# Optimization experiments

Measured on AMD Instinct MI355X. Metric: run time of the kernel, lower is better.

The kernel has to match this reference:

```python
import jax, jax.numpy as jnp
import numpy as np

T = 10.0            # neuralef_loss_cfg['t']
ALPHA = 0.05        # neuralef_loss_cfg['alpha']
PW_W = 0.1          # pixelwise_adj_weight
PW_DIV = 1.0        # pixelwise_adj_div_factor
K_LIST = ((20, 2.0), (10, 0.1))  # hard-coded in source


def _pdist(x):
    # x: (b, n, d) -> (b, n, n) euclidean distance (torch.cdist)
    sq = jnp.sum(x * x, -1)
    d2 = sq[:, :, None] + sq[:, None, :] - 2.0 * jnp.einsum('bnd,bmd->bnm', x, x)
    return jnp.sqrt(jnp.maximum(d2, 0.0))


def _mutual_knn(feats, k):
    # mutual k-NN boolean adjacency: scatter topk then AND with transpose
    bs, n, _ = feats.shape
    neg = -_pdist(feats)
    neg = jnp.where(jnp.eye(n, dtype=bool), -jnp.inf, neg)
    idx = jax.lax.top_k(neg, k)[1]                       # (bs, n, k)
    res = jnp.zeros((bs, n, n), dtype=bool).at[
        jnp.arange(bs)[:, None, None], jnp.arange(n)[None, :, None], idx].set(True)
    return jnp.logical_and(res, res.transpose(0, 2, 1))


def setup_inputs() -> dict:
    key = jax.random.key(0)
    k1, k2, k3 = jax.random.split(key, 3)
    N, C, K = 8192, 384, 512
    bs, h, w = 8, 32, 32
    FF = jax.random.normal(k1, (N, C), dtype=jnp.float32)
    Psi = jax.random.normal(k2, (N, K), dtype=jnp.float32)
    im = jax.random.uniform(k3, (bs, 3, h, w), dtype=jnp.float32, minval=-1.0, maxval=1.0)
    return {"FF": FF, "Psi": Psi, "im": im}


def reference(FF, Psi, im):
    N = FF.shape[0]
    Psi = Psi * (T / N)
    # --- adjacency (torch.no_grad block) ---
    FFn = FF / jnp.linalg.norm(FF, axis=1, keepdims=True)
    A = FFn @ FFn.T
    A = jnp.where(jnp.eye(N, dtype=bool), 0.0, A)       # fill_diagonal_(0)
    A = jnp.maximum(A, 0.0)                              # thresholded kernel
    # --- pixelwise mutual-kNN adjacency per image ---
    bs, _, h, w = im.shape
    hw = h * w
    im01 = (im + 1.0) * 0.5
    x_ = jnp.tile(jnp.linspace(0.0, 1.0, w), h)          # (hw,)
    y_ = jnp.repeat(jnp.linspace(0.0, 1.0, h), w)        # (hw,)
    feat = im01.reshape(bs, 3, hw).transpose(0, 2, 1) / PW_DIV  # (bs, hw, 3)
    A_p = None
    for k, dw in K_LIST:
        f2 = jnp.concatenate([
            feat,
            jnp.broadcast_to((x_ * dw)[None, :, None], (bs, hw, 1)),
            jnp.broadcast_to((y_ * dw)[None, :, None], (bs, hw, 1)),
        ], -1)
        m = _mutual_knn(f2, k)
        A_p = m if A_p is None else jnp.logical_or(A_p, m)
    # add PW_W * A_p to block-diagonal blocks of A
    A4 = A.reshape(bs, hw, bs, hw)
    bi = jnp.arange(bs)
    A4 = A4.at[bi, :, bi, :].add(PW_W * A_p.astype(A.dtype))
    A = A4.reshape(N, N)
    # degree normalization
    D = jax.lax.rsqrt(A.sum(-1) / (N - 1))
    gram = A * D[None, :] * D[:, None]
    # --- neuralef loss ---
    R = Psi.T @ gram @ Psi                               # (K, K)
    R_hat = jax.lax.stop_gradient(Psi).T @ gram @ Psi    # no_sg=False
    loss = -jnp.trace(R)
    reg = jnp.sum(jnp.triu(R_hat ** 2, 1)) * ALPHA
    return jnp.stack([loss, reg])
```

## Files before the change

### kernel.cpp

```cpp
#include <hip/hip_runtime.h>
#include <hip/hip_bf16.h>

#define NN 8192
#define CC 384
#define KD 512
#define HWP 1024

typedef __attribute__((ext_vector_type(8))) short bf16x8;
typedef __attribute__((ext_vector_type(4))) float f32x4;

static constexpr float T_OVER_N = 10.0f / 8192.0f;

__device__ __forceinline__ float bf2f(unsigned short u) {
    union { unsigned int i; float f; } x;
    x.i = ((unsigned int)u) << 16;
    return x.f;
}
__device__ __forceinline__ unsigned short f2bf(float f) {
    __hip_bfloat16 h = __float2bfloat16(f);
    unsigned short u;
    __builtin_memcpy(&u, &h, sizeof(u));
    return u;
}

__device__ __forceinline__ void wait_vm8() {
    asm volatile("s_waitcnt vmcnt(8)" ::: "memory");
    __builtin_amdgcn_sched_barrier(0);
}
__device__ __forceinline__ void wait_vm0() {
    asm volatile("s_waitcnt vmcnt(0)" ::: "memory");
    __builtin_amdgcn_sched_barrier(0);
}
__device__ __forceinline__ void rawbar() {
    __builtin_amdgcn_s_barrier();
    __builtin_amdgcn_sched_barrier(0);
}

__device__ __forceinline__ void stage_tile(const unsigned short* __restrict__ src, long ld,
                                           int k0, unsigned short* lds) {
    const int t = threadIdx.x;
    #pragma unroll
    for (int i = 0; i < 4; ++i) {
        int slot = i * 256 + t;
        int row = slot >> 3;
        int cl = (slot & 7) ^ (row & 7);
        const unsigned short* g = src + (long)row * ld + k0 + cl * 8;
        __builtin_amdgcn_global_load_lds((const __attribute__((address_space(1))) void*)g,
                                         (__attribute__((address_space(3))) void*)(lds + (size_t)slot * 8),
                                         16, 0, 0);
    }
}

__device__ __forceinline__ bf16x8 read_frag(const unsigned short* lds, int r, int chunk) {
    int byte = (r << 7) + (((chunk ^ r) & 7) << 4) + ((chunk & ~7) << 4);
    return *(const bf16x8*)((const char*)lds + byte);
}

__device__ __forceinline__ void gemm_step(const unsigned short* As, const unsigned short* Bs,
                                          int arl, int brl, int lhi, f32x4 (&acc)[4][4]) {
    #pragma unroll
    for (int ks = 0; ks < 2; ++ks) {
        bf16x8 a[4], b[4];
        #pragma unroll
        for (int m = 0; m < 4; ++m) a[m] = read_frag(As, arl + m * 16, ks * 4 + lhi);
        #pragma unroll
        for (int n = 0; n < 4; ++n) b[n] = read_frag(Bs, brl + n * 16, ks * 4 + lhi);
        #pragma unroll
        for (int m = 0; m < 4; ++m)
            #pragma unroll
            for (int n = 0; n < 4; ++n)
                acc[m][n] = __builtin_amdgcn_mfma_f32_16x16x32_bf16(a[m], b[n], acc[m][n], 0, 0, 0);
    }
}

__global__ __launch_bounds__(128) void k_normalize(const float* __restrict__ FF,
                                                   unsigned short* __restrict__ FFnb) {
    int row = blockIdx.x;
    int tid = threadIdx.x;
    const float* src = FF + (size_t)row * CC;
    float v0 = src[tid], v1 = src[tid + 128], v2 = src[tid + 256];
    float s = v0 * v0 + v1 * v1 + v2 * v2;
    #pragma unroll
    for (int off = 32; off > 0; off >>= 1) s += __shfl_down(s, off, 64);
    __shared__ float ls[2];
    if ((tid & 63) == 0) ls[tid >> 6] = s;
    __syncthreads();
    float inv = 1.0f / sqrtf(ls[0] + ls[1]);
    unsigned short* dst = FFnb + (size_t)row * CC;
    dst[tid] = f2bf(v0 * inv);
    dst[tid + 128] = f2bf(v1 * inv);
    dst[tid + 256] = f2bf(v2 * inv);
}

__global__ __launch_bounds__(256) void k_knn(const float* __restrict__ im,
                                             unsigned char* __restrict__ res20,
                                             unsigned char* __restrict__ res10) {
    const int lane = threadIdx.x & 63;
    const int id = blockIdx.x * 4 + (threadIdx.x >> 6);
    const int v = id & 1;
    const int rest = id >> 1;
    const int p = rest & 1023;
    const int b = rest >> 10;
    const float dw = v ? 0.1f : 2.0f;
    const int kneigh = v ? 10 : 20;
    const float* im0 = im + (size_t)b * 3 * HWP;
    const float scale = dw * (1.0f / 31.0f);
    float rf0 = (im0[p] + 1.f) * 0.5f;
    float rf1 = (im0[HWP + p] + 1.f) * 0.5f;
    float rf2 = (im0[2 * HWP + p] + 1.f) * 0.5f;
    float rx = (float)(p & 31) * scale;
    float ry = (float)(p >> 5) * scale;
    unsigned int key[16];
    #pragma unroll
    for (int e = 0; e < 16; ++e) {
        int q = e * 64 + lane;
        float f0 = (im0[q] + 1.f) * 0.5f - rf0;
        float f1 = (im0[HWP + q] + 1.f) * 0.5f - rf1;
        float f2 = (im0[2 * HWP + q] + 1.f) * 0.5f - rf2;
        float fx = (float)(q & 31) * scale - rx;
        float fy = (float)(q >> 5) * scale - ry;
        float d = f0 * f0 + f1 * f1 + f2 * f2 + fx * fx + fy * fy;
        unsigned int db = __float_as_uint(d);
        key[e] = (q == p) ? 0xFFFFFFFFu : ((db & 0xFFFFFC00u) | (unsigned int)q);
    }
    unsigned int selmask = 0;
    for (int it = 0; it < kneigh; ++it) {
        unsigned int m = key[0];
        #pragma unroll
        for (int e = 1; e < 16; ++e) m = (key[e] < m) ? key[e] : m;
        #pragma unroll
        for (int off = 1; off < 64; off <<= 1) {
            unsigned int o = __shfl_xor(m, off, 64);
            m = (o < m) ? o : m;
        }
        int q = (int)(m & 1023u);
        if ((q & 63) == lane) {
            int e = q >> 6;
            selmask |= 1u << e;
            key[e] = 0xFFFFFFFFu;
        }
    }
    unsigned char* dst = (v ? res10 : res20) + ((size_t)(b * HWP + p)) * HWP;
    #pragma unroll
    for (int e = 0; e < 16; ++e) dst[e * 64 + lane] = (unsigned char)((selmask >> e) & 1u);
}

__global__ __launch_bounds__(256, 2) void k_gram_off(const unsigned short* __restrict__ FFnb,
                                                     unsigned short* __restrict__ A,
                                                     float* __restrict__ rowsum) {
    __shared__ __align__(16) unsigned short Sh[4][8192];
    int s = ((blockIdx.x & 7) * 260) + (blockIdx.x >> 3);
    int ti = 0, rem = s;
    while (rem >= 64 - ti) { rem -= 64 - ti; ++ti; }
    const int tj = ti + rem;
    if ((ti >> 3) == (tj >> 3)) return;
    const int row0 = ti * 128, col0 = tj * 128;
    const int tid = threadIdx.x, l = tid & 63, wid = tid >> 6;
    const int wr = (wid >> 1) * 64, wc = (wid & 1) * 64;
    const int arl = wr + (l & 15), brl = wc + (l & 15), lhi = l >> 4;
    f32x4 z = {0.f, 0.f, 0.f, 0.f};
    f32x4 acc[4][4];
    #pragma unroll
    for (int m = 0; m < 4; ++m)
        #pragma unroll
        for (int n = 0; n < 4; ++n) acc[m][n] = z;

    stage_tile(FFnb + (long)row0 * CC, CC, 0, Sh[0]);
    stage_tile(FFnb + (long)col0 * CC, CC, 0, Sh[1]);
    for (int t = 0; t < 6; ++t) {
        const int cur = t & 1, nxt = cur ^ 1;
        if (t + 1 < 6) {
            stage_tile(FFnb + (long)row0 * CC, CC, (t + 1) * 64, Sh[2 * nxt]);
            stage_tile(FFnb + (long)col0 * CC, CC, (t + 1) * 64, Sh[2 * nxt + 1]);
            wait_vm8();
        } else {
            wait_vm0();
        }
        rawbar();
        gemm_step(Sh[2 * cur], Sh[2 * cur + 1], arl, brl, lhi, acc);
        rawbar();
    }
    float rs[4][4];
    float cs[4] = {0.f, 0.f, 0.f, 0.f};
    #pragma unroll
    for (int m = 0; m < 4; ++m)
        #pragma unroll
        for (int r = 0; r < 4; ++r) rs[m][r] = 0.f;
    char* Mir = (char*)Sh;
    #pragma unroll
    for (int m = 0; m < 4; ++m) {
        #pragma unroll
        for (int n = 0; n < 4; ++n) {
            #pragma unroll
            for (int r = 0; r < 4; ++r) {
                int il = wr + m * 16 + lhi * 4 + r;
                int jl = wc + n * 16 + (l & 15);
                float vv = fmaxf(acc[m][n][r], 0.f);
                unsigned short u = f2bf(vv);
                A[(long)(row0 + il) * NN + col0 + jl] = u;
                rs[m][r] += vv;
                cs[n] += vv;
                *(unsigned short*)(Mir + jl * 256 + ((il * 2) ^ ((jl & 15) << 4))) = u;
            }
        }
    }
    #pragma unroll
    for (int m = 0; m < 4; ++m)
        #pragma unroll
        for (int r = 0; r < 4; ++r) {
            float p = rs[m][r];
            #pragma unroll
            for (int off = 1; off < 16; off <<= 1) p += __shfl_xor(p, off, 64);
            if ((l & 15) == 0) atomicAdd(&rowsum[row0 + wr + m * 16 + lhi * 4 + r], p);
        }
    #pragma unroll
    for (int n = 0; n < 4; ++n) {
        float p = cs[n];
        p += __shfl_xor(p, 16, 64);
        p += __shfl_xor(p, 32, 64);
        if (l < 16) atomicAdd(&rowsum[col0 + wc + n * 16 + l], p);
    }
    __syncthreads();
    #pragma unroll
    for (int p8 = 0; p8 < 8; ++p8) {
        int idx = p8 * 256 + tid;
        int jl = idx >> 4;
        int cl = idx & 15;
        int sl = cl ^ (jl & 15);
        bf16x8 v = *(const bf16x8*)(Mir + jl * 256 + sl * 16);
        *(bf16x8*)(A + (long)(col0 + jl) * NN + row0 + cl * 8) = v;
    }
}

__global__ __launch_bounds__(256, 2) void k_gram_diag(const unsigned short* __restrict__ FFnb,
                                                      const unsigned char* __restrict__ res20,
                                                      const unsigned char* __restrict__ res10,
                                                      unsigned short* __restrict__ A,
                                                      float* __restrict__ rowsum) {
    __shared__ __align__(16) unsigned short Sh[4][8192];
    int s = ((blockIdx.x & 7) * 36) + (blockIdx.x >> 3);
    int band = s / 36, p = s % 36;
    int a = 0, rem = p;
    while (rem >= 8 - a) { rem -= 8 - a; ++a; }
    const int ti = band * 8 + a, tj = band * 8 + a + rem;
    const int row0 = ti * 128, col0 = tj * 128;
    const int tid = threadIdx.x, l = tid & 63, wid = tid >> 6;
    const int wr = (wid >> 1) * 64, wc = (wid & 1) * 64;
    const int arl = wr + (l & 15), brl = wc + (l & 15), lhi = l >> 4;
    f32x4 z = {0.f, 0.f, 0.f, 0.f};
    f32x4 acc[4][4];
    #pragma unroll
    for (int m = 0; m < 4; ++m)
        #pragma unroll
        for (int n = 0; n < 4; ++n) acc[m][n] = z;

    stage_tile(FFnb + (long)row0 * CC, CC, 0, Sh[0]);
    stage_tile(FFnb + (long)col0 * CC, CC, 0, Sh[1]);
    for (int t = 0; t < 6; ++t) {
        const int cur = t & 1, nxt = cur ^ 1;
        if (t + 1 < 6) {
            stage_tile(FFnb + (long)row0 * CC, CC, (t + 1) * 64, Sh[2 * nxt]);
            stage_tile(FFnb + (long)col0 * CC, CC, (t + 1) * 64, Sh[2 * nxt + 1]);
            wait_vm8();
        } else {
            wait_vm0();
        }
        rawbar();
        gemm_step(Sh[2 * cur], Sh[2 * cur + 1], arl, brl, lhi, acc);
        rawbar();
    }
    const bool offd = (ti != tj);
    const long mbase = ((long)band) << 20;
    float rs[4][4];
    float cs[4] = {0.f, 0.f, 0.f, 0.f};
    #pragma unroll
    for (int m = 0; m < 4; ++m)
        #pragma unroll
        for (int r = 0; r < 4; ++r) rs[m][r] = 0.f;
    char* Mir = (char*)Sh;
    #pragma unroll
    for (int m = 0; m < 4; ++m) {
        #pragma unroll
        for (int n = 0; n < 4; ++n) {
            #pragma unroll
            for (int r = 0; r < 4; ++r) {
                int il = wr + m * 16 + lhi * 4 + r;
                int jl = wc + n * 16 + (l & 15);
                int gi = row0 + il, gj = col0 + jl;
                float vv = acc[m][n][r];
                vv = (gi == gj) ? 0.f : fmaxf(vv, 0.f);
                int li = gi & 1023, lj = gj & 1023;
                unsigned char mm = (unsigned char)(
                    (res20[mbase + (long)li * HWP + lj] & res20[mbase + (long)lj * HWP + li]) |
                    (res10[mbase + (long)li * HWP + lj] & res10[mbase + (long)lj * HWP + li]));
                vv += 0.1f * (float)mm;
                unsigned short u = f2bf(vv);
                A[(long)gi * NN + gj] = u;
                rs[m][r] += vv;
                if (offd) {
                    cs[n] += vv;
                    *(unsigned short*)(Mir + jl * 256 + ((il * 2) ^ ((jl & 15) << 4))) = u;
                }
            }
        }
    }
    #pragma unroll
    for (int m = 0; m < 4; ++m)
        #pragma unroll
        for (int r = 0; r < 4; ++r) {
            float p2 = rs[m][r];
            #pragma unroll
            for (int off = 1; off < 16; off <<= 1) p2 += __shfl_xor(p2, off, 64);
            if ((l & 15) == 0) atomicAdd(&rowsum[row0 + wr + m * 16 + lhi * 4 + r], p2);
        }
    if (offd) {
        #pragma unroll
        for (int n = 0; n < 4; ++n) {
            float p2 = cs[n];
            p2 += __shfl_xor(p2, 16, 64);
            p2 += __shfl_xor(p2, 32, 64);
            if (l < 16) atomicAdd(&rowsum[col0 + wc + n * 16 + l], p2);
        }
        __syncthreads();
        #pragma unroll
        for (int p8 = 0; p8 < 8; ++p8) {
            int idx = p8 * 256 + tid;
            int jl = idx >> 4;
            int cl = idx & 15;
            int sl = cl ^ (jl & 15);
            bf16x8 v = *(const bf16x8*)(Mir + jl * 256 + sl * 16);
            *(bf16x8*)(A + (long)(col0 + jl) * NN + row0 + cl * 8) = v;
        }
    }
}

__global__ __launch_bounds__(256) void k_d(const float* __restrict__ rowsum,
                                           float* __restrict__ Dv) {
    int i = blockIdx.x * 256 + threadIdx.x;
    Dv[i] = 1.0f / sqrtf(rowsum[i] * (1.0f / 8191.0f));
}

__global__ __launch_bounds__(256) void k_psiT(const float* __restrict__ Psi,
                                              const float* __restrict__ Dv,
                                              unsigned short* __restrict__ PaT,
                                              unsigned short* __restrict__ PsT) {
    __shared__ unsigned short tile[128][72];
    __shared__ float Dvs[64];
    const int j0 = blockIdx.x * 64;
    const int n0 = blockIdx.y * 128;
    const int t = threadIdx.x;
    if (t < 64) Dvs[t] = Dv[j0 + t];
    #pragma unroll
    for (int i = 0; i < 8; ++i) {
        int jl = i * 8 + (t >> 5);
        int c4 = (t & 31) * 4;
        float4 vv = *(const float4*)(Psi + (size_t)(j0 + jl) * KD + n0 + c4);
        tile[c4 + 0][jl] = f2bf(vv.x * T_OVER_N);
        tile[c4 + 1][jl] = f2bf(vv.y * T_OVER_N);
        tile[c4 + 2][jl] = f2bf(vv.z * T_OVER_N);
        tile[c4 + 3][jl] = f2bf(vv.w * T_OVER_N);
    }
    __syncthreads();
    const int nl = t >> 1;
    const int jh = (t & 1) * 32;
    unsigned short pa[32], ps[32];
    #pragma unroll
    for (int jj = 0; jj < 32; ++jj) {
        unsigned short u = tile[nl][jh + jj];
        pa[jj] = u;
        ps[jj] = f2bf(bf2f(u) * Dvs[jh + jj]);
    }
    unsigned short* dpa = PaT + (size_t)(n0 + nl) * NN + j0 + jh;
    unsigned short* dps = PsT + (size_t)(n0 + nl) * NN + j0 + jh;
    #pragma unroll
    for (int c = 0; c < 4; ++c) {
        *(bf16x8*)(dpa + c * 8) = *(const bf16x8*)(pa + c * 8);
        *(bf16x8*)(dps + c * 8) = *(const bf16x8*)(ps + c * 8);
    }
}

__global__ __launch_bounds__(256, 2) void k_yt5(const unsigned short* __restrict__ A,
                                                const unsigned short* __restrict__ PsT,
                                                unsigned short* __restrict__ Wpart) {
    __shared__ __align__(16) unsigned short Sh[4][8192];
    int slot = (blockIdx.x & 7) * 64 + (blockIdx.x >> 3);
    const int it = slot >> 3;
    const int sub = slot & 7;
    const int nt = sub & 3, kz = sub >> 2;
    const int row0 = it * 128, col0 = nt * 128;
    const int tid = threadIdx.x, l = tid & 63, wid = tid >> 6;
    const int wr = (wid >> 1) * 64, wc = (wid & 1) * 64;
    const int arl = wr + (l & 15), brl = wc + (l & 15), lhi = l >> 4;
    f32x4 z = {0.f, 0.f, 0.f, 0.f};
    f32x4 acc[4][4];
    #pragma unroll
    for (int m = 0; m < 4; ++m)
        #pragma unroll
        for (int n = 0; n < 4; ++n) acc[m][n] = z;

    const unsigned short* Abase = A + (long)row0 * NN;
    const unsigned short* Bbase = PsT + (long)col0 * NN;
    const int kbeg = kz * 4096;
    stage_tile(Abase, NN, kbeg, Sh[0]);
    stage_tile(Bbase, NN, kbeg, Sh[1]);
    for (int t = 0; t < 64; ++t) {
        const int cur = t & 1, nxt = cur ^ 1;
        if (t + 1 < 64) {
            int k1 = kbeg + (t + 1) * 64;
            stage_tile(Abase, NN, k1, Sh[2 * nxt]);
            stage_tile(Bbase, NN, k1, Sh[2 * nxt + 1]);
            wait_vm8();
        } else {
            wait_vm0();
        }
        rawbar();
        gemm_step(Sh[2 * cur], Sh[2 * cur + 1], arl, brl, lhi, acc);
        rawbar();
    }
    unsigned short* Wp = Wpart + (long)kz * NN * KD;
    #pragma unroll
    for (int m = 0; m < 4; ++m) {
        #pragma unroll
        for (int r = 0; r < 4; ++r) {
            int gi = row0 + wr + m * 16 + lhi * 4 + r;
            #pragma unroll
            for (int n = 0; n < 4; ++n) {
                int gj = col0 + wc + n * 16 + (l & 15);
                Wp[(long)gi * KD + gj] = f2bf(acc[m][n][r]);
            }
        }
    }
}

__global__ __launch_bounds__(256) void k_comb(const unsigned short* __restrict__ Wpart,
                                              const float* __restrict__ Dv,
                                              unsigned short* __restrict__ YT) {
    __shared__ unsigned short t64[64][80];
    const int i0 = blockIdx.x * 64;
    const int n0 = blockIdx.y * 64;
    const int t = threadIdx.x;
    int il = t >> 2, nc = (t & 3) * 16;
    const unsigned short* p0 = Wpart + (long)(i0 + il) * KD + n0 + nc;
    const unsigned short* p1 = p0 + (long)NN * KD;
    bf16x8 a0 = *(const bf16x8*)p0;
    bf16x8 a1 = *(const bf16x8*)(p0 + 8);
    bf16x8 b0 = *(const bf16x8*)p1;
    bf16x8 b1 = *(const bf16x8*)(p1 + 8);
    float dvi = Dv[i0 + il];
    #pragma unroll
    for (int e = 0; e < 8; ++e) {
        t64[nc + e][il]     = f2bf((bf2f((unsigned short)a0[e]) + bf2f((unsigned short)b0[e])) * dvi);
        t64[nc + 8 + e][il] = f2bf((bf2f((unsigned short)a1[e]) + bf2f((unsigned short)b1[e])) * dvi);
    }
    __syncthreads();
    int nl = t >> 2, jc = (t & 3) * 16;
    bf16x8 o0 = *(const bf16x8*)(&t64[nl][jc]);
    bf16x8 o1 = *(const bf16x8*)(&t64[nl][jc + 8]);
    *(bf16x8*)(YT + (long)(n0 + nl) * NN + i0 + jc) = o0;
    *(bf16x8*)(YT + (long)(n0 + nl) * NN + i0 + jc + 8) = o1;
}

__global__ __launch_bounds__(256, 2) void k_r(const unsigned short* __restrict__ PaT,
                                              const unsigned short* __restrict__ YT,
                                              float* __restrict__ R) {
    static const int t1tab[10] = {0,0,0,0,1,1,1,2,2,3};
    static const int t2tab[10] = {0,1,2,3,1,2,3,2,3,3};
    const int t1 = t1tab[blockIdx.x], t2 = t2tab[blockIdx.x], kz = blockIdx.y;
    __shared__ __align__(16) unsigned short Sh[4][8192];
    const int row0 = t1 * 128, col0 = t2 * 128;
    const int tid = threadIdx.x, l = tid & 63, wid = tid >> 6;
    const int wr = (wid >> 1) * 64, wc = (wid & 1) * 64;
    const int arl = wr + (l & 15), brl = wc + (l & 15), lhi = l >> 4;
    f32x4 z = {0.f, 0.f, 0.f, 0.f};
    f32x4 acc[4][4];
    #pragma unroll
    for (int m = 0; m < 4; ++m)
        #pragma unroll
        for (int n = 0; n < 4; ++n) acc[m][n] = z;

    const int kbeg = kz * 512;
    stage_tile(PaT + (long)row0 * NN, NN, kbeg, Sh[0]);
    stage_tile(YT + (long)col0 * NN, NN, kbeg, Sh[1]);
    for (int t = 0; t < 8; ++t) {
        const int cur = t & 1, nxt = cur ^ 1;
        if (t + 1 < 8) {
            int k1 = kbeg + (t + 1) * 64;
            stage_tile(PaT + (long)row0 * NN, NN, k1, Sh[2 * nxt]);
            stage_tile(YT + (long)col0 * NN, NN, k1, Sh[2 * nxt + 1]);
            wait_vm8();
        } else {
            wait_vm0();
        }
        rawbar();
        gemm_step(Sh[2 * cur], Sh[2 * cur + 1], arl, brl, lhi, acc);
        rawbar();
    }
    #pragma unroll
    for (int m = 0; m < 4; ++m) {
        #pragma unroll
        for (int n = 0; n < 4; ++n) {
            #pragma unroll
            for (int r = 0; r < 4; ++r) {
                int gk1 = row0 + wr + m * 16 + lhi * 4 + r;
                int gk2 = col0 + wc + n * 16 + (l & 15);
                atomicAdd(&R[(long)gk1 * KD + gk2], acc[m][n][r]);
            }
        }
    }
}

__global__ __launch_bounds__(256) void k_tri(const float* __restrict__ R,
                                             float* __restrict__ acc2) {
    float tr = 0.f, rg = 0.f;
    for (int idx = blockIdx.x * 256 + threadIdx.x; idx < KD * KD; idx += 64 * 256) {
        int k1 = idx >> 9, k2 = idx & 511;
        float v = R[idx];
        if (k1 == k2) tr += v;
        else if (k1 < k2) rg += v * v;
    }
    #pragma unroll
    for (int off = 32; off > 0; off >>= 1) {
        tr += __shfl_down(tr, off, 64);
        rg += __shfl_down(rg, off, 64);
    }
    __shared__ float lt[4], lr[4];
    int tid = threadIdx.x;
    if ((tid & 63) == 0) { lt[tid >> 6] = tr; lr[tid >> 6] = rg; }
    __syncthreads();
    if (tid == 0) {
        atomicAdd(&acc2[0], lt[0] + lt[1] + lt[2] + lt[3]);
        atomicAdd(&acc2[1], lr[0] + lr[1] + lr[2] + lr[3]);
    }
}

__global__ void k_fin(const float* __restrict__ acc2, float* __restrict__ out) {
    out[0] = -acc2[0];
    out[1] = 0.05f * acc2[1];
}

extern "C" void kernel_launch(void* const* d_in, const int* in_sizes, int n_in,
                              void* d_out, int out_size, void* d_ws, size_t ws_size,
                              hipStream_t stream) {
    const float* FF  = (const float*)d_in[0];
    const float* Psi = (const float*)d_in[1];
    const float* im  = (const float*)d_in[2];
    float* out = (float*)d_out;
    char* ws = (char*)d_ws;
    size_t off = 0;
    auto alloc = [&](size_t bytes) {
        size_t o = off;
        off += (bytes + 255) & ~(size_t)255;
        return o;
    };
    unsigned short* FFnb  = (unsigned short*)(ws + alloc((size_t)NN * CC * 2));
    unsigned char* res20  = (unsigned char*)(ws + alloc((size_t)8 * HWP * HWP));
    unsigned char* res10  = (unsigned char*)(ws + alloc((size_t)8 * HWP * HWP));
    float* rowsum         = (float*)(ws + alloc((size_t)NN * 4));
    float* Dv             = (float*)(ws + alloc((size_t)NN * 4));
    unsigned short* PaT   = (unsigned short*)(ws + alloc((size_t)KD * NN * 2));
    unsigned short* PsT   = (unsigned short*)(ws + alloc((size_t)KD * NN * 2));
    unsigned short* Wpart = (unsigned short*)(ws + alloc((size_t)2 * NN * KD * 2));
    unsigned short* YT    = (unsigned short*)(ws + alloc((size_t)KD * NN * 2));
    float* R              = (float*)(ws + alloc((size_t)KD * KD * 4));
    float* acc2           = (float*)(ws + alloc(256));
    unsigned short* A     = (unsigned short*)(ws + alloc((size_t)NN * NN * 2));

    hipMemsetAsync(rowsum, 0, (size_t)NN * 4, stream);
    hipMemsetAsync(R, 0, (size_t)KD * KD * 4, stream);
    hipMemsetAsync(acc2, 0, 8, stream);

    k_normalize<<<NN, 128, 0, stream>>>(FF, FFnb);
    k_knn<<<4096, 256, 0, stream>>>(im, res20, res10);
    k_gram_off<<<2080, 256, 0, stream>>>(FFnb, A, rowsum);
    k_gram_diag<<<288, 256, 0, stream>>>(FFnb, res20, res10, A, rowsum);
    k_d<<<NN / 256, 256, 0, stream>>>(rowsum, Dv);
    k_psiT<<<dim3(128, 4), 256, 0, stream>>>(Psi, Dv, PaT, PsT);
    k_yt5<<<512, 256, 0, stream>>>(A, PsT, Wpart);
    k_comb<<<dim3(NN / 64, KD / 64), 256, 0, stream>>>(Wpart, Dv, YT);
    k_r<<<dim3(10, 16), 256, 0, stream>>>(PaT, YT, R);
    k_tri<<<64, 256, 0, stream>>>(R, acc2);
    k_fin<<<1, 1, 0, stream>>>(acc2, out);
}
```

Before: 292.4 us.

## Halve gram kernel LDS to raise occupancy and stage both A tile stores

Cuts shared memory in both gram kernels from four to two bf16 tiles by dropping double buffering of the K-loop, and raises the launch bound to 4 blocks per CU. The direct tile store to A, which was scattered as 2-byte writes, now goes through LDS and is written out as coalesced 16-byte vectors, like the mirrored transpose tile. The aim is better latency hiding from more resident waves plus cheaper global writes. In exchange, load latency inside each block is no longer overlapped with MFMA work, and the epilogue gains extra barriers and LDS passes.

New measurement: 327.7 us. +12.1%, slower.

```diff
diff --git a/kernel.cpp b/kernel.cpp
--- a/kernel.cpp
+++ b/kernel.cpp
@@ -145,10 +145,10 @@
     for (int e = 0; e < 16; ++e) dst[e * 64 + lane] = (unsigned char)((selmask >> e) & 1u);
 }
 
-__global__ __launch_bounds__(256, 2) void k_gram_off(const unsigned short* __restrict__ FFnb,
+__global__ __launch_bounds__(256, 4) void k_gram_off(const unsigned short* __restrict__ FFnb,
                                                      unsigned short* __restrict__ A,
                                                      float* __restrict__ rowsum) {
-    __shared__ __align__(16) unsigned short Sh[4][8192];
+    __shared__ __align__(16) unsigned short Sh[2][8192];
     int s = ((blockIdx.x & 7) * 260) + (blockIdx.x >> 3);
     int ti = 0, rem = s;
     while (rem >= 64 - ti) { rem -= 64 - ti; ++ti; }
@@ -165,19 +165,12 @@
         #pragma unroll
         for (int n = 0; n < 4; ++n) acc[m][n] = z;
 
-    stage_tile(FFnb + (long)row0 * CC, CC, 0, Sh[0]);
-    stage_tile(FFnb + (long)col0 * CC, CC, 0, Sh[1]);
     for (int t = 0; t < 6; ++t) {
-        const int cur = t & 1, nxt = cur ^ 1;
-        if (t + 1 < 6) {
-            stage_tile(FFnb + (long)row0 * CC, CC, (t + 1) * 64, Sh[2 * nxt]);
-            stage_tile(FFnb + (long)col0 * CC, CC, (t + 1) * 64, Sh[2 * nxt + 1]);
-            wait_vm8();
-        } else {
-            wait_vm0();
-        }
-        rawbar();
-        gemm_step(Sh[2 * cur], Sh[2 * cur + 1], arl, brl, lhi, acc);
+        stage_tile(FFnb + (long)row0 * CC, CC, t * 64, Sh[0]);
+        stage_tile(FFnb + (long)col0 * CC, CC, t * 64, Sh[1]);
+        wait_vm0();
+        rawbar();
+        gemm_step(Sh[0], Sh[1], arl, brl, lhi, acc);
         rawbar();
     }
     float rs[4][4];
@@ -186,7 +179,7 @@
     for (int m = 0; m < 4; ++m)
         #pragma unroll
         for (int r = 0; r < 4; ++r) rs[m][r] = 0.f;
-    char* Mir = (char*)Sh;
+    char* Buf = (char*)Sh;
     #pragma unroll
     for (int m = 0; m < 4; ++m) {
         #pragma unroll
@@ -196,11 +189,9 @@
                 int il = wr + m * 16 + lhi * 4 + r;
                 int jl = wc + n * 16 + (l & 15);
                 float vv = fmaxf(acc[m][n][r], 0.f);
-                unsigned short u = f2bf(vv);
-                A[(long)(row0 + il) * NN + col0 + jl] = u;
                 rs[m][r] += vv;
                 cs[n] += vv;
-                *(unsigned short*)(Mir + jl * 256 + ((il * 2) ^ ((jl & 15) << 4))) = u;
+                *(unsigned short*)(Buf + il * 256 + ((jl * 2) ^ ((il & 15) << 4))) = f2bf(vv);
             }
         }
     }
@@ -224,20 +215,44 @@
     #pragma unroll
     for (int p8 = 0; p8 < 8; ++p8) {
         int idx = p8 * 256 + tid;
+        int il = idx >> 4;
+        int cl = idx & 15;
+        int sl = cl ^ (il & 15);
+        bf16x8 v = *(const bf16x8*)(Buf + il * 256 + sl * 16);
+        *(bf16x8*)(A + (long)(row0 + il) * NN + col0 + cl * 8) = v;
+    }
+    __syncthreads();
+    #pragma unroll
+    for (int m = 0; m < 4; ++m) {
+        #pragma unroll
+        for (int n = 0; n < 4; ++n) {
+            #pragma unroll
+            for (int r = 0; r < 4; ++r) {
+                int il = wr + m * 16 + lhi * 4 + r;
+                int jl = wc + n * 16 + (l & 15);
+                float vv = fmaxf(acc[m][n][r], 0.f);
+                *(unsigned short*)(Buf + jl * 256 + ((il * 2) ^ ((jl & 15) << 4))) = f2bf(vv);
+            }
+        }
+    }
+    __syncthreads();
+    #pragma unroll
+    for (int p8 = 0; p8 < 8; ++p8) {
+        int idx = p8 * 256 + tid;
         int jl = idx >> 4;
         int cl = idx & 15;
         int sl = cl ^ (jl & 15);
-        bf16x8 v = *(const bf16x8*)(Mir + jl * 256 + sl * 16);
+        bf16x8 v = *(const bf16x8*)(Buf + jl * 256 + sl * 16);
         *(bf16x8*)(A + (long)(col0 + jl) * NN + row0 + cl * 8) = v;
     }
 }
 
-__global__ __launch_bounds__(256, 2) void k_gram_diag(const unsigned short* __restrict__ FFnb,
+__global__ __launch_bounds__(256, 4) void k_gram_diag(const unsigned short* __restrict__ FFnb,
                                                       const unsigned char* __restrict__ res20,
                                                       const unsigned char* __restrict__ res10,
                                                       unsigned short* __restrict__ A,
                                                       float* __restrict__ rowsum) {
-    __shared__ __align__(16) unsigned short Sh[4][8192];
+    __shared__ __align__(16) unsigned short Sh[2][8192];
     int s = ((blockIdx.x & 7) * 36) + (blockIdx.x >> 3);
     int band = s / 36, p = s % 36;
     int a = 0, rem = p;
@@ -254,19 +269,12 @@
         #pragma unroll
         for (int n = 0; n < 4; ++n) acc[m][n] = z;
 
-    stage_tile(FFnb + (long)row0 * CC, CC, 0, Sh[0]);
-    stage_tile(FFnb + (long)col0 * CC, CC, 0, Sh[1]);
     for (int t = 0; t < 6; ++t) {
-        const int cur = t & 1, nxt = cur ^ 1;
-        if (t + 1 < 6) {
-            stage_tile(FFnb + (long)row0 * CC, CC, (t + 1) * 64, Sh[2 * nxt]);
-            stage_tile(FFnb + (long)col0 * CC, CC, (t + 1) * 64, Sh[2 * nxt + 1]);
-            wait_vm8();
-        } else {
-            wait_vm0();
-        }
-        rawbar();
-        gemm_step(Sh[2 * cur], Sh[2 * cur + 1], arl, brl, lhi, acc);
+        stage_tile(FFnb + (long)row0 * CC, CC, t * 64, Sh[0]);
+        stage_tile(FFnb + (long)col0 * CC, CC, t * 64, Sh[1]);
+        wait_vm0();
+        rawbar();
+        gemm_step(Sh[0], Sh[1], arl, brl, lhi, acc);
         rawbar();
     }
     const bool offd = (ti != tj);
@@ -277,7 +285,7 @@
     for (int m = 0; m < 4; ++m)
         #pragma unroll
         for (int r = 0; r < 4; ++r) rs[m][r] = 0.f;
-    char* Mir = (char*)Sh;
+    char* Buf = (char*)Sh;
     #pragma unroll
     for (int m = 0; m < 4; ++m) {
         #pragma unroll
@@ -294,13 +302,10 @@
                     (res20[mbase + (long)li * HWP + lj] & res20[mbase + (long)lj * HWP + li]) |
                     (res10[mbase + (long)li * HWP + lj] & res10[mbase + (long)lj * HWP + li]));
                 vv += 0.1f * (float)mm;
-                unsigned short u = f2bf(vv);
-                A[(long)gi * NN + gj] = u;
+                acc[m][n][r] = vv;
                 rs[m][r] += vv;
-                if (offd) {
-                    cs[n] += vv;
-                    *(unsigned short*)(Mir + jl * 256 + ((il * 2) ^ ((jl & 15) << 4))) = u;
-                }
+                if (offd) cs[n] += vv;
+                *(unsigned short*)(Buf + il * 256 + ((jl * 2) ^ ((il & 15) << 4))) = f2bf(vv);
             }
         }
     }
@@ -321,6 +326,31 @@
             p2 += __shfl_xor(p2, 32, 64);
             if (l < 16) atomicAdd(&rowsum[col0 + wc + n * 16 + l], p2);
         }
+    }
+    __syncthreads();
+    #pragma unroll
+    for (int p8 = 0; p8 < 8; ++p8) {
+        int idx = p8 * 256 + tid;
+        int il = idx >> 4;
+        int cl = idx & 15;
+        int sl = cl ^ (il & 15);
+        bf16x8 v = *(const bf16x8*)(Buf + il * 256 + sl * 16);
+        *(bf16x8*)(A + (long)(row0 + il) * NN + col0 + cl * 8) = v;
+    }
+    if (offd) {
+        __syncthreads();
+        #pragma unroll
+        for (int m = 0; m < 4; ++m) {
+            #pragma unroll
+            for (int n = 0; n < 4; ++n) {
+                #pragma unroll
+                for (int r = 0; r < 4; ++r) {
+                    int il = wr + m * 16 + lhi * 4 + r;
+                    int jl = wc + n * 16 + (l & 15);
+                    *(unsigned short*)(Buf + jl * 256 + ((il * 2) ^ ((jl & 15) << 4))) = f2bf(acc[m][n][r]);
+                }
+            }
+        }
         __syncthreads();
         #pragma unroll
         for (int p8 = 0; p8 < 8; ++p8) {
@@ -328,7 +358,7 @@
             int jl = idx >> 4;
             int cl = idx & 15;
             int sl = cl ^ (jl & 15);
-            bf16x8 v = *(const bf16x8*)(Mir + jl * 256 + sl * 16);
+            bf16x8 v = *(const bf16x8*)(Buf + jl * 256 + sl * 16);
             *(bf16x8*)(A + (long)(col0 + jl) * NN + row0 + cl * 8) = v;
         }
     }
```
